# Performance work log

Measured on AMD Instinct MI355X. Metric: run time of the kernel, lower is better.

The kernel has to match this reference:

```python
import jax, jax.numpy as jnp
import numpy as np

HEADS = 4
EPS = 1e-5

def _layernorm(x, g, b):
    mu = jnp.mean(x, axis=-1, keepdims=True)
    var = jnp.var(x, axis=-1, keepdims=True)
    return (x - mu) / jnp.sqrt(var + EPS) * g + b

def setup_inputs() -> dict:
    key = jax.random.key(0)
    ks = jax.random.split(key, 16)
    N, dim, k, G = 400000, 256, 1, 4096
    h = jax.random.normal(ks[0], (N, dim), dtype=jnp.float32)
    batch = jnp.sort(jax.random.randint(ks[1], (N,), 0, G).astype(jnp.int64))
    s = 1.0 / np.sqrt(dim)
    return {
        "h": h,
        "batch": batch,
        "num_graphs": G,
        "seed": jax.random.normal(ks[2], (k, dim), dtype=jnp.float32),
        "in_proj_w": jax.random.uniform(ks[3], (3 * dim, dim), minval=-s, maxval=s, dtype=jnp.float32),
        "in_proj_b": jnp.zeros((3 * dim,), jnp.float32),
        "out_w": jax.random.uniform(ks[4], (dim, dim), minval=-s, maxval=s, dtype=jnp.float32),
        "out_b": jnp.zeros((dim,), jnp.float32),
        "w1": jax.random.uniform(ks[5], (4 * dim, dim), minval=-s, maxval=s, dtype=jnp.float32),
        "b1": jnp.zeros((4 * dim,), jnp.float32),
        "w2": jax.random.uniform(ks[6], (dim, 4 * dim), minval=-1.0 / np.sqrt(4 * dim), maxval=1.0 / np.sqrt(4 * dim), dtype=jnp.float32),
        "b2": jnp.zeros((dim,), jnp.float32),
        "g1": jnp.ones((dim,), jnp.float32),
        "beta1": jnp.zeros((dim,), jnp.float32),
        "g2": jnp.ones((dim,), jnp.float32),
        "beta2": jnp.zeros((dim,), jnp.float32),
    }

def reference(h, batch, num_graphs, seed, in_proj_w, in_proj_b, out_w, out_b,
              w1, b1, w2, b2, g1, beta1, g2, beta2):
    N, dim = h.shape
    k = seed.shape[0]
    hd = dim // HEADS
    G = num_graphs
    # q/k/v projections (torch MHA packed in_proj: rows [0:dim]=Q, [dim:2dim]=K, [2dim:]=V)
    q = seed @ in_proj_w[:dim].T + in_proj_b[:dim]                 # [k, dim]
    kk = h @ in_proj_w[dim:2 * dim].T + in_proj_b[dim:2 * dim]     # [N, dim]
    vv = h @ in_proj_w[2 * dim:].T + in_proj_b[2 * dim:]           # [N, dim]
    qh = q.reshape(k, HEADS, hd).transpose(1, 0, 2)                # [H, k, hd]
    kh = kk.reshape(N, HEADS, hd)                                  # [N, H, hd]
    vh = vv.reshape(N, HEADS, hd)                                  # [N, H, hd]
    scale = 1.0 / np.sqrt(hd)
    scores = jnp.einsum('hkd,nhd->nhk', qh, kh) * scale            # [N, H, k]
    # segment softmax over nodes of each graph
    smax = jax.ops.segment_max(scores, batch, num_segments=G)      # [G, H, k]
    e = jnp.exp(scores - smax[batch])                              # [N, H, k]
    denom = jax.ops.segment_sum(e, batch, num_segments=G)          # [G, H, k]
    wv = jax.ops.segment_sum(e[:, :, :, None] * vh[:, :, None, :], batch, num_segments=G)  # [G, H, k, hd]
    attn = jnp.where(denom[..., None] > 0, wv / jnp.maximum(denom, 1e-9)[..., None], 0.0)
    attn = attn.transpose(0, 2, 1, 3).reshape(G, k, dim)           # [G, k, dim]
    o = attn @ out_w.T + out_b                                     # [G, k, dim]
    x = _layernorm(o + seed[None, :, :], g1, beta1)
    f = jax.nn.relu(x @ w1.T + b1) @ w2.T + b2
    x = _layernorm(x + f, g2, beta2)
    # empty graphs output zeros (matches torch loop)
    count = jax.ops.segment_sum(jnp.ones((N,), jnp.float32), batch, num_segments=G)
    return jnp.where((count > 0)[:, None, None], x, 0.0)
```

## Files before the change

kernel.cpp:

```cpp
#include <hip/hip_runtime.h>
#include <hip/hip_bf16.h>


#define DIM 256
#define CHUNK 16

typedef short bf16x8 __attribute__((ext_vector_type(8)));
typedef float f32x4  __attribute__((ext_vector_type(4)));
#define MFMA16(a, b, c) __builtin_amdgcn_mfma_f32_16x16x32_bf16(a, b, c, 0, 0, 0)

#define GLOAD_LDS16(gp, lp)                                          \
    __builtin_amdgcn_global_load_lds(                                \
        (const __attribute__((address_space(1))) void*)(gp),         \
        (__attribute__((address_space(3))) void*)(lp), 16, 0, 0)

#define OFF_C      0
#define OFF_D      1024
#define OFF_CONST  1040
#define OFF_P2B    2048
#define OFF_W1B    133120
#define OFF_W2B    264192
#define OFF_TB     395264
#define OFF_CNT    6162432
#define OFF_STARTS 6166528

__global__ __launch_bounds__(256) void prep_all_kernel(
    const float* __restrict__ seed, const float* __restrict__ ipw,
    const float* __restrict__ ipb, const float* __restrict__ out_w,
    const float* __restrict__ out_b, const float* __restrict__ w1,
    const float* __restrict__ w2, const int* __restrict__ batch,
    float* __restrict__ cvec, float* __restrict__ dconst,
    float* __restrict__ constvec, __hip_bfloat16* __restrict__ P2b,
    __hip_bfloat16* __restrict__ w1b, __hip_bfloat16* __restrict__ w2b,
    int* __restrict__ starts, int N, int G)
{
    int b = blockIdx.x, t = threadIdx.x;
    __shared__ float q_s[DIM];
    if (b < 1024) {
        int i = b >> 2, hD = b & 3;
        float a = 0.f;
        for (int j = 0; j < 64; ++j)
            a += out_w[i * DIM + hD * 64 + j]
               * ipw[(size_t)(2 * DIM + hD * 64 + j) * DIM + t];
        P2b[(size_t)i * 1024 + hD * DIM + t] = __float2bfloat16(a);
    } else if (b == 1024) {
        const float scale = 0.125f;
        float acc = ipb[t];
        for (int d = 0; d < DIM; ++d) acc += seed[d] * ipw[t * DIM + d];
        q_s[t] = acc;
        __syncthreads();
        for (int hh = 0; hh < 4; ++hh) {
            float a = 0.f;
            for (int j = 0; j < 64; ++j)
                a += q_s[hh * 64 + j] * ipw[(size_t)(DIM + hh * 64 + j) * DIM + t];
            cvec[hh * DIM + t] = a * scale;
        }
        if (t < 4) {
            float a = 0.f;
            for (int j = 0; j < 64; ++j)
                a += q_s[t * 64 + j] * ipb[DIM + t * 64 + j];
            dconst[t] = a * scale;
        }
        float cc = out_b[t];
        for (int c = 0; c < DIM; ++c)
            cc += out_w[t * DIM + c] * ipb[2 * DIM + c];
        constvec[t] = cc;
    } else if (b < 1153) {
        int base = (b - 1025) * 2048 + t;
        for (int i = 0; i < 8; ++i)
            w1b[base + i * 256] = __float2bfloat16(w1[base + i * 256]);
    } else if (b < 1281) {
        int base = (b - 1153) * 2048 + t;
        for (int i = 0; i < 8; ++i)
            w2b[base + i * 256] = __float2bfloat16(w2[base + i * 256]);
    } else {
        int n = (b - 1281) * 256 + t;
        if (n < N) {
            int bn = batch[n];
            int bp = (n == 0) ? -1 : batch[n - 1];
            for (int gg = bp + 1; gg <= bn; ++gg) starts[gg] = n;
            if (n == N - 1)
                for (int gg = bn + 1; gg <= G; ++gg) starts[gg] = N;
        }
    }
}

__global__ __launch_bounds__(256) void attn_pool_kernel(
    const float* __restrict__ hmat, const int* __restrict__ starts,
    const float* __restrict__ cvec, const float* __restrict__ dconst,
    __hip_bfloat16* __restrict__ Tb, int* __restrict__ cnt)
{
    int g = blockIdx.x;
    int tid = threadIdx.x;
    int lane = tid & 63, wave = tid >> 6;

    __shared__ float hbuf[2][CHUNK][DIM];
    __shared__ float lred[4][4];

    int s = starts[g], e = starts[g + 1];
    if (tid == 0) cnt[g] = e - s;
    size_t tbase = (size_t)g * 1024;
    if (e == s) {
        __hip_bfloat16 z = __float2bfloat16(0.f);
        Tb[tbase + tid] = z; Tb[tbase + 256 + tid] = z;
        Tb[tbase + 512 + tid] = z; Tb[tbase + 768 + tid] = z;
        return;
    }

    int hh = lane & 3, seg = lane >> 2;
    const float* cb = cvec + hh * DIM + seg * 16;
    float4 cr0 = *(const float4*)(cb + 0);
    float4 cr1 = *(const float4*)(cb + 4);
    float4 cr2 = *(const float4*)(cb + 8);
    float4 cr3 = *(const float4*)(cb + 12);
    float dc_mine = dconst[hh];

    float S00 = 0.f, S01 = 0.f, S02 = 0.f, S03 = 0.f;
    float S10 = 0.f, S11 = 0.f, S12 = 0.f, S13 = 0.f;
    float S20 = 0.f, S21 = 0.f, S22 = 0.f, S23 = 0.f;
    float S30 = 0.f, S31 = 0.f, S32 = 0.f, S33 = 0.f;
    float lp = 0.f;

    {
        int c0 = min(CHUNK, e - s);
#pragma unroll
        for (int i = 0; i < 4; ++i) {
            int r = wave * 4 + i;
            if (r < c0)
                GLOAD_LDS16(&hmat[(size_t)(s + r) * DIM + lane * 4],
                            &hbuf[0][r][0]);
        }
    }

    int cur = 0;
    for (int n0 = s; n0 < e; n0 += CHUNK, cur ^= 1) {
        int ccnt = min(CHUNK, e - n0);
        __syncthreads();

        int n1 = n0 + CHUNK;
        if (n1 < e) {
            int cn = min(CHUNK, e - n1);
#pragma unroll
            for (int i = 0; i < 4; ++i) {
                int r = wave * 4 + i;
                if (r < cn)
                    GLOAD_LDS16(&hmat[(size_t)(n1 + r) * DIM + lane * 4],
                                &hbuf[cur ^ 1][r][0]);
            }
        }

        for (int j = wave; j < ccnt; j += 4) {
            const float* hb = &hbuf[cur][j][0];
            const float* hs = hb + seg * 16;
            float4 h0 = *(const float4*)(hs + 0);
            float4 h1 = *(const float4*)(hs + 4);
            float4 h2 = *(const float4*)(hs + 8);
            float4 h3 = *(const float4*)(hs + 12);
            float p = h0.x * cr0.x + h0.y * cr0.y + h0.z * cr0.z + h0.w * cr0.w
                    + h1.x * cr1.x + h1.y * cr1.y + h1.z * cr1.z + h1.w * cr1.w
                    + h2.x * cr2.x + h2.y * cr2.y + h2.z * cr2.z + h2.w * cr2.w
                    + h3.x * cr3.x + h3.y * cr3.y + h3.z * cr3.z + h3.w * cr3.w;
            p += __shfl_xor(p, 4);
            p += __shfl_xor(p, 8);
            p += __shfl_xor(p, 16);
            p += __shfl_xor(p, 32);
            float ev = __expf(p + dc_mine);
            lp += ev;
            float e0 = __shfl(ev, 0), e1 = __shfl(ev, 1);
            float e2 = __shfl(ev, 2), e3 = __shfl(ev, 3);
            float v0 = hb[lane], v1 = hb[64 + lane];
            float v2 = hb[128 + lane], v3 = hb[192 + lane];
            S00 = fmaf(e0, v0, S00); S01 = fmaf(e0, v1, S01);
            S02 = fmaf(e0, v2, S02); S03 = fmaf(e0, v3, S03);
            S10 = fmaf(e1, v0, S10); S11 = fmaf(e1, v1, S11);
            S12 = fmaf(e1, v2, S12); S13 = fmaf(e1, v3, S13);
            S20 = fmaf(e2, v0, S20); S21 = fmaf(e2, v1, S21);
            S22 = fmaf(e2, v2, S22); S23 = fmaf(e2, v3, S23);
            S30 = fmaf(e3, v0, S30); S31 = fmaf(e3, v1, S31);
            S32 = fmaf(e3, v2, S32); S33 = fmaf(e3, v3, S33);
        }
    }

    __syncthreads();
    float* part = &hbuf[0][0][0];
#define PIDX(w_, h_, c_) ((((w_) * 4 + (h_)) * 4 + (c_)) * 64 + lane)
    part[PIDX(wave, 0, 0)] = S00; part[PIDX(wave, 0, 1)] = S01;
    part[PIDX(wave, 0, 2)] = S02; part[PIDX(wave, 0, 3)] = S03;
    part[PIDX(wave, 1, 0)] = S10; part[PIDX(wave, 1, 1)] = S11;
    part[PIDX(wave, 1, 2)] = S12; part[PIDX(wave, 1, 3)] = S13;
    part[PIDX(wave, 2, 0)] = S20; part[PIDX(wave, 2, 1)] = S21;
    part[PIDX(wave, 2, 2)] = S22; part[PIDX(wave, 2, 3)] = S23;
    part[PIDX(wave, 3, 0)] = S30; part[PIDX(wave, 3, 1)] = S31;
    part[PIDX(wave, 3, 2)] = S32; part[PIDX(wave, 3, 3)] = S33;
#undef PIDX
    if (lane < 4) lred[wave][lane] = lp;
    __syncthreads();

    int cg = tid >> 6, ln = tid & 63;
#pragma unroll
    for (int h = 0; h < 4; ++h) {
        int base = (h * 4 + cg) * 64 + ln;
        float sum = part[base] + part[base + 1024]
                  + part[base + 2048] + part[base + 3072];
        float den = lred[0][h] + lred[1][h] + lred[2][h] + lred[3][h];
        Tb[tbase + h * 256 + tid] = __float2bfloat16(sum / den);
    }
}

__global__ __launch_bounds__(256) void mlp_fused_kernel(
    const __hip_bfloat16* __restrict__ Tb, const __hip_bfloat16* __restrict__ P2b,
    const float* __restrict__ constvec, const float* __restrict__ seed,
    const float* __restrict__ g1, const float* __restrict__ be1,
    const __hip_bfloat16* __restrict__ w1b, const float* __restrict__ b1,
    const __hip_bfloat16* __restrict__ w2b, const float* __restrict__ b2,
    const float* __restrict__ g2, const float* __restrict__ be2,
    const int* __restrict__ cnt, float* __restrict__ outp)
{
    int m0 = blockIdx.x * 16;
    int tid = threadIdx.x;
    int w = tid >> 6, lane = tid & 63, quad = lane >> 4, l16 = lane & 15;

    __shared__ float x1s[16][260];
    __shared__ __hip_bfloat16 x1bs[16][264];
    __shared__ __hip_bfloat16 us[16][1032];
    __shared__ float redS[4][16], redQ[4][16];

    f32x4 acc0[4];
#pragma unroll
    for (int i = 0; i < 4; ++i) acc0[i] = (f32x4){0.f, 0.f, 0.f, 0.f};
    const __hip_bfloat16* Ap0 = Tb + (size_t)(m0 + l16) * 1024 + quad * 8;
    const __hip_bfloat16* Bp0 = P2b + (size_t)(w * 64 + l16) * 1024 + quad * 8;
    for (int k0 = 0; k0 < 1024; k0 += 32) {
        bf16x8 a = *(const bf16x8*)(Ap0 + k0);
#pragma unroll
        for (int nt = 0; nt < 4; ++nt) {
            bf16x8 b = *(const bf16x8*)(Bp0 + (size_t)nt * 16 * 1024 + k0);
            acc0[nt] = MFMA16(a, b, acc0[nt]);
        }
    }
    float v0[4][4];
    {
        float sum[4] = {0, 0, 0, 0}, sq[4] = {0, 0, 0, 0};
#pragma unroll
        for (int nt = 0; nt < 4; ++nt) {
            int col = w * 64 + nt * 16 + l16;
            float cv = constvec[col] + seed[col];
#pragma unroll
            for (int r = 0; r < 4; ++r) {
                float x = acc0[nt][r] + cv;
                v0[nt][r] = x; sum[r] += x; sq[r] += x * x;
            }
        }
#pragma unroll
        for (int r = 0; r < 4; ++r) {
            float s_ = sum[r], q_ = sq[r];
            s_ += __shfl_xor(s_, 1);  q_ += __shfl_xor(q_, 1);
            s_ += __shfl_xor(s_, 2);  q_ += __shfl_xor(q_, 2);
            s_ += __shfl_xor(s_, 4);  q_ += __shfl_xor(q_, 4);
            s_ += __shfl_xor(s_, 8);  q_ += __shfl_xor(q_, 8);
            if (l16 == 0) { redS[w][quad * 4 + r] = s_; redQ[w][quad * 4 + r] = q_; }
        }
    }
    __syncthreads();
    {
        float mu_r[4], rs_r[4];
#pragma unroll
        for (int r = 0; r < 4; ++r) {
            int row = quad * 4 + r;
            float s_ = redS[0][row] + redS[1][row] + redS[2][row] + redS[3][row];
            float q_ = redQ[0][row] + redQ[1][row] + redQ[2][row] + redQ[3][row];
            float mu = s_ * (1.f / 256);
            float var = q_ * (1.f / 256) - mu * mu;
            mu_r[r] = mu;
            rs_r[r] = rsqrtf(fmaxf(var, 0.f) + 1e-5f);
        }
#pragma unroll
        for (int nt = 0; nt < 4; ++nt) {
            int col = w * 64 + nt * 16 + l16;
            float gg = g1[col], bb = be1[col];
#pragma unroll
            for (int r = 0; r < 4; ++r) {
                int row = quad * 4 + r;
                float y = (v0[nt][r] - mu_r[r]) * rs_r[r] * gg + bb;
                x1s[row][col] = y;
                x1bs[row][col] = __float2bfloat16(y);
            }
        }
    }
    __syncthreads();

    f32x4 acc1[16];
#pragma unroll
    for (int i = 0; i < 16; ++i) acc1[i] = (f32x4){0.f, 0.f, 0.f, 0.f};
    const __hip_bfloat16* Bp1 = w1b + (size_t)(w * 256 + l16) * 256 + quad * 8;
#pragma unroll
    for (int k0 = 0; k0 < 256; k0 += 32) {
        bf16x8 a = *(const bf16x8*)&x1bs[l16][quad * 8 + k0];
#pragma unroll
        for (int nt = 0; nt < 16; ++nt) {
            bf16x8 b = *(const bf16x8*)(Bp1 + (size_t)nt * 16 * 256 + k0);
            acc1[nt] = MFMA16(a, b, acc1[nt]);
        }
    }
#pragma unroll
    for (int nt = 0; nt < 16; ++nt) {
        int col = w * 256 + nt * 16 + l16;
        float bb = b1[col];
#pragma unroll
        for (int r = 0; r < 4; ++r) {
            int row = quad * 4 + r;
            us[row][col] = __float2bfloat16(fmaxf(acc1[nt][r] + bb, 0.f));
        }
    }
    __syncthreads();

    f32x4 acc2[4];
#pragma unroll
    for (int i = 0; i < 4; ++i) acc2[i] = (f32x4){0.f, 0.f, 0.f, 0.f};
    const __hip_bfloat16* Bp2 = w2b + (size_t)(w * 64 + l16) * 1024 + quad * 8;
    for (int k0 = 0; k0 < 1024; k0 += 32) {
        bf16x8 a = *(const bf16x8*)&us[l16][quad * 8 + k0];
#pragma unroll
        for (int nt = 0; nt < 4; ++nt) {
            bf16x8 b = *(const bf16x8*)(Bp2 + (size_t)nt * 16 * 1024 + k0);
            acc2[nt] = MFMA16(a, b, acc2[nt]);
        }
    }
    float v2[4][4];
    {
        float sum[4] = {0, 0, 0, 0}, sq[4] = {0, 0, 0, 0};
#pragma unroll
        for (int nt = 0; nt < 4; ++nt) {
            int col = w * 64 + nt * 16 + l16;
            float bb = b2[col];
#pragma unroll
            for (int r = 0; r < 4; ++r) {
                int row = quad * 4 + r;
                float x = acc2[nt][r] + bb + x1s[row][col];
                v2[nt][r] = x; sum[r] += x; sq[r] += x * x;
            }
        }
#pragma unroll
        for (int r = 0; r < 4; ++r) {
            float s_ = sum[r], q_ = sq[r];
            s_ += __shfl_xor(s_, 1);  q_ += __shfl_xor(q_, 1);
            s_ += __shfl_xor(s_, 2);  q_ += __shfl_xor(q_, 2);
            s_ += __shfl_xor(s_, 4);  q_ += __shfl_xor(q_, 4);
            s_ += __shfl_xor(s_, 8);  q_ += __shfl_xor(q_, 8);
            if (l16 == 0) { redS[w][quad * 4 + r] = s_; redQ[w][quad * 4 + r] = q_; }
        }
    }
    __syncthreads();
    {
#pragma unroll
        for (int r = 0; r < 4; ++r) {
            int row = quad * 4 + r;
            float s_ = redS[0][row] + redS[1][row] + redS[2][row] + redS[3][row];
            float q_ = redQ[0][row] + redQ[1][row] + redQ[2][row] + redQ[3][row];
            float mu = s_ * (1.f / 256);
            float var = q_ * (1.f / 256) - mu * mu;
            float rs = rsqrtf(fmaxf(var, 0.f) + 1e-5f);
            int gr = m0 + row;
            float mask = (cnt[gr] > 0) ? 1.f : 0.f;
#pragma unroll
            for (int nt = 0; nt < 4; ++nt) {
                int col = w * 64 + nt * 16 + l16;
                float y = ((v2[nt][r] - mu) * rs * g2[col] + be2[col]) * mask;
                outp[(size_t)gr * 256 + col] = y;
            }
        }
    }
}

extern "C" void kernel_launch(void* const* d_in, const int* in_sizes, int n_in,
                              void* d_out, int out_size, void* d_ws, size_t ws_size,
                              hipStream_t stream) {
    const float* h     = (const float*)d_in[0];
    const int*   batch = (const int*)d_in[1];
    const float* seed  = (const float*)d_in[3];
    const float* ipw   = (const float*)d_in[4];
    const float* ipb   = (const float*)d_in[5];
    const float* out_w = (const float*)d_in[6];
    const float* out_b = (const float*)d_in[7];
    const float* w1    = (const float*)d_in[8];
    const float* b1    = (const float*)d_in[9];
    const float* w2    = (const float*)d_in[10];
    const float* b2    = (const float*)d_in[11];
    const float* g1    = (const float*)d_in[12];
    const float* be1   = (const float*)d_in[13];
    const float* g2    = (const float*)d_in[14];
    const float* be2   = (const float*)d_in[15];

    int N = in_sizes[1];
    int G = out_size / DIM;

    float* ws = (float*)d_ws;
    float* cvec     = ws + OFF_C;
    float* dconst   = ws + OFF_D;
    float* constvec = ws + OFF_CONST;
    __hip_bfloat16* P2b = (__hip_bfloat16*)(ws + OFF_P2B);
    __hip_bfloat16* w1b = (__hip_bfloat16*)(ws + OFF_W1B);
    __hip_bfloat16* w2b = (__hip_bfloat16*)(ws + OFF_W2B);
    __hip_bfloat16* Tb  = (__hip_bfloat16*)(ws + OFF_TB);
    int*   cnt      = (int*)(ws + OFF_CNT);
    int*   startsp  = (int*)(ws + OFF_STARTS);

    int sblocks = (N + 255) / 256;
    prep_all_kernel<<<1281 + sblocks, 256, 0, stream>>>(
        seed, ipw, ipb, out_w, out_b, w1, w2, batch,
        cvec, dconst, constvec, P2b, w1b, w2b, startsp, N, G);
    attn_pool_kernel<<<G, 256, 0, stream>>>(h, startsp, cvec, dconst, Tb, cnt);
    mlp_fused_kernel<<<G / 16, 256, 0, stream>>>(Tb, P2b, constvec, seed, g1, be1,
                                                 w1b, b1, w2b, b2, g2, be2, cnt,
                                                 (float*)d_out);
}
```

Baseline: 663.7 us.

## Use per-wave private LDS buffers in attention pool, widen MLP block to 16 waves

The attention pooling kernel now gives each wave its own double-buffered LDS rows. It issues next-chunk loads unconditionally, clamping row indices, and waits with s_waitcnt vmcnt instead of block-wide __syncthreads, which removes barrier stalls in the streaming loop. The MLP kernel goes from 4 to 16 waves per block, each computing a narrower slice of columns, to raise parallelism and latency hiding for the small 256-block grid. The costs are redundant clamped loads on tail chunks, reliance on manual waitcnt correctness, and larger LayerNorm cross-wave reductions over 16 partials.

```diff
diff --git a/kernel.cpp b/kernel.cpp
--- a/kernel.cpp
+++ b/kernel.cpp
@@ -94,7 +94,7 @@
     int tid = threadIdx.x;
     int lane = tid & 63, wave = tid >> 6;
 
-    __shared__ float hbuf[2][CHUNK][DIM];
+    __shared__ float hbuf[4][2][4][DIM];
     __shared__ float lred[4][4];
 
     int s = starts[g], e = starts[g + 1];
@@ -121,36 +121,30 @@
     float S30 = 0.f, S31 = 0.f, S32 = 0.f, S33 = 0.f;
     float lp = 0.f;
 
-    {
-        int c0 = min(CHUNK, e - s);
-#pragma unroll
-        for (int i = 0; i < 4; ++i) {
-            int r = wave * 4 + i;
-            if (r < c0)
-                GLOAD_LDS16(&hmat[(size_t)(s + r) * DIM + lane * 4],
-                            &hbuf[0][r][0]);
-        }
+    int rows0 = wave * 4;
+
+#pragma unroll
+    for (int i = 0; i < 4; ++i) {
+        int r = min(s + rows0 + i, e - 1);
+        GLOAD_LDS16(&hmat[(size_t)r * DIM + lane * 4], &hbuf[wave][0][i][0]);
     }
 
     int cur = 0;
     for (int n0 = s; n0 < e; n0 += CHUNK, cur ^= 1) {
         int ccnt = min(CHUNK, e - n0);
-        __syncthreads();
-
         int n1 = n0 + CHUNK;
-        if (n1 < e) {
-            int cn = min(CHUNK, e - n1);
-#pragma unroll
-            for (int i = 0; i < 4; ++i) {
-                int r = wave * 4 + i;
-                if (r < cn)
-                    GLOAD_LDS16(&hmat[(size_t)(n1 + r) * DIM + lane * 4],
-                                &hbuf[cur ^ 1][r][0]);
-            }
-        }
-
-        for (int j = wave; j < ccnt; j += 4) {
-            const float* hb = &hbuf[cur][j][0];
+#pragma unroll
+        for (int i = 0; i < 4; ++i) {
+            int r = min(n1 + rows0 + i, e - 1);
+            GLOAD_LDS16(&hmat[(size_t)r * DIM + lane * 4],
+                        &hbuf[wave][cur ^ 1][i][0]);
+        }
+        asm volatile("s_waitcnt vmcnt(4)" ::: "memory");
+        __builtin_amdgcn_sched_barrier(0);
+
+        int nmine = min(max(ccnt - rows0, 0), 4);
+        for (int j = 0; j < nmine; ++j) {
+            const float* hb = &hbuf[wave][cur][j][0];
             const float* hs = hb + seg * 16;
             float4 h0 = *(const float4*)(hs + 0);
             float4 h1 = *(const float4*)(hs + 4);
@@ -181,8 +175,10 @@
         }
     }
 
-    __syncthreads();
-    float* part = &hbuf[0][0][0];
+    asm volatile("s_waitcnt vmcnt(0)" ::: "memory");
+    __builtin_amdgcn_sched_barrier(0);
+    __syncthreads();
+    float* part = &hbuf[0][0][0][0];
 #define PIDX(w_, h_, c_) ((((w_) * 4 + (h_)) * 4 + (c_)) * 64 + lane)
     part[PIDX(wave, 0, 0)] = S00; part[PIDX(wave, 0, 1)] = S01;
     part[PIDX(wave, 0, 2)] = S02; part[PIDX(wave, 0, 3)] = S03;
@@ -207,7 +203,7 @@
     }
 }
 
-__global__ __launch_bounds__(256) void mlp_fused_kernel(
+__global__ __launch_bounds__(1024) void mlp_fused_kernel(
     const __hip_bfloat16* __restrict__ Tb, const __hip_bfloat16* __restrict__ P2b,
     const float* __restrict__ constvec, const float* __restrict__ seed,
     const float* __restrict__ g1, const float* __restrict__ be1,
@@ -223,33 +219,26 @@
     __shared__ float x1s[16][260];
     __shared__ __hip_bfloat16 x1bs[16][264];
     __shared__ __hip_bfloat16 us[16][1032];
-    __shared__ float redS[4][16], redQ[4][16];
-
-    f32x4 acc0[4];
-#pragma unroll
-    for (int i = 0; i < 4; ++i) acc0[i] = (f32x4){0.f, 0.f, 0.f, 0.f};
+    __shared__ float redS[16][16], redQ[16][16];
+
+    f32x4 acc0 = (f32x4){0.f, 0.f, 0.f, 0.f};
     const __hip_bfloat16* Ap0 = Tb + (size_t)(m0 + l16) * 1024 + quad * 8;
-    const __hip_bfloat16* Bp0 = P2b + (size_t)(w * 64 + l16) * 1024 + quad * 8;
+    const __hip_bfloat16* Bp0 = P2b + (size_t)(w * 16 + l16) * 1024 + quad * 8;
+#pragma unroll 4
     for (int k0 = 0; k0 < 1024; k0 += 32) {
         bf16x8 a = *(const bf16x8*)(Ap0 + k0);
-#pragma unroll
-        for (int nt = 0; nt < 4; ++nt) {
-            bf16x8 b = *(const bf16x8*)(Bp0 + (size_t)nt * 16 * 1024 + k0);
-            acc0[nt] = MFMA16(a, b, acc0[nt]);
-        }
-    }
-    float v0[4][4];
+        bf16x8 b = *(const bf16x8*)(Bp0 + k0);
+        acc0 = MFMA16(a, b, acc0);
+    }
+    float v0[4];
     {
-        float sum[4] = {0, 0, 0, 0}, sq[4] = {0, 0, 0, 0};
-#pragma unroll
-        for (int nt = 0; nt < 4; ++nt) {
-            int col = w * 64 + nt * 16 + l16;
-            float cv = constvec[col] + seed[col];
-#pragma unroll
-            for (int r = 0; r < 4; ++r) {
-                float x = acc0[nt][r] + cv;
-                v0[nt][r] = x; sum[r] += x; sq[r] += x * x;
-            }
+        int col = w * 16 + l16;
+        float cv = constvec[col] + seed[col];
+        float sum[4], sq[4];
+#pragma unroll
+        for (int r = 0; r < 4; ++r) {
+            float x = acc0[r] + cv;
+            v0[r] = x; sum[r] = x; sq[r] = x * x;
         }
 #pragma unroll
         for (int r = 0; r < 4; ++r) {
@@ -267,44 +256,42 @@
 #pragma unroll
         for (int r = 0; r < 4; ++r) {
             int row = quad * 4 + r;
-            float s_ = redS[0][row] + redS[1][row] + redS[2][row] + redS[3][row];
-            float q_ = redQ[0][row] + redQ[1][row] + redQ[2][row] + redQ[3][row];
+            float s_ = 0.f, q_ = 0.f;
+#pragma unroll
+            for (int ww = 0; ww < 16; ++ww) { s_ += redS[ww][row]; q_ += redQ[ww][row]; }
             float mu = s_ * (1.f / 256);
             float var = q_ * (1.f / 256) - mu * mu;
             mu_r[r] = mu;
             rs_r[r] = rsqrtf(fmaxf(var, 0.f) + 1e-5f);
         }
-#pragma unroll
-        for (int nt = 0; nt < 4; ++nt) {
-            int col = w * 64 + nt * 16 + l16;
-            float gg = g1[col], bb = be1[col];
-#pragma unroll
-            for (int r = 0; r < 4; ++r) {
-                int row = quad * 4 + r;
-                float y = (v0[nt][r] - mu_r[r]) * rs_r[r] * gg + bb;
-                x1s[row][col] = y;
-                x1bs[row][col] = __float2bfloat16(y);
-            }
-        }
-    }
-    __syncthreads();
-
-    f32x4 acc1[16];
-#pragma unroll
-    for (int i = 0; i < 16; ++i) acc1[i] = (f32x4){0.f, 0.f, 0.f, 0.f};
-    const __hip_bfloat16* Bp1 = w1b + (size_t)(w * 256 + l16) * 256 + quad * 8;
+        int col = w * 16 + l16;
+        float gg = g1[col], bb = be1[col];
+#pragma unroll
+        for (int r = 0; r < 4; ++r) {
+            int row = quad * 4 + r;
+            float y = (v0[r] - mu_r[r]) * rs_r[r] * gg + bb;
+            x1s[row][col] = y;
+            x1bs[row][col] = __float2bfloat16(y);
+        }
+    }
+    __syncthreads();
+
+    f32x4 acc1[4];
+#pragma unroll
+    for (int i = 0; i < 4; ++i) acc1[i] = (f32x4){0.f, 0.f, 0.f, 0.f};
+    const __hip_bfloat16* Bp1 = w1b + (size_t)(w * 64 + l16) * 256 + quad * 8;
 #pragma unroll
     for (int k0 = 0; k0 < 256; k0 += 32) {
         bf16x8 a = *(const bf16x8*)&x1bs[l16][quad * 8 + k0];
 #pragma unroll
-        for (int nt = 0; nt < 16; ++nt) {
+        for (int nt = 0; nt < 4; ++nt) {
             bf16x8 b = *(const bf16x8*)(Bp1 + (size_t)nt * 16 * 256 + k0);
             acc1[nt] = MFMA16(a, b, acc1[nt]);
         }
     }
 #pragma unroll
-    for (int nt = 0; nt < 16; ++nt) {
-        int col = w * 256 + nt * 16 + l16;
+    for (int nt = 0; nt < 4; ++nt) {
+        int col = w * 64 + nt * 16 + l16;
         float bb = b1[col];
 #pragma unroll
         for (int r = 0; r < 4; ++r) {
@@ -314,31 +301,24 @@
     }
     __syncthreads();
 
-    f32x4 acc2[4];
-#pragma unroll
-    for (int i = 0; i < 4; ++i) acc2[i] = (f32x4){0.f, 0.f, 0.f, 0.f};
-    const __hip_bfloat16* Bp2 = w2b + (size_t)(w * 64 + l16) * 1024 + quad * 8;
+    f32x4 acc2 = (f32x4){0.f, 0.f, 0.f, 0.f};
+    const __hip_bfloat16* Bp2 = w2b + (size_t)(w * 16 + l16) * 1024 + quad * 8;
+#pragma unroll 4
     for (int k0 = 0; k0 < 1024; k0 += 32) {
         bf16x8 a = *(const bf16x8*)&us[l16][quad * 8 + k0];
-#pragma unroll
-        for (int nt = 0; nt < 4; ++nt) {
-            bf16x8 b = *(const bf16x8*)(Bp2 + (size_t)nt * 16 * 1024 + k0);
-            acc2[nt] = MFMA16(a, b, acc2[nt]);
-        }
-    }
-    float v2[4][4];
+        bf16x8 b = *(const bf16x8*)(Bp2 + k0);
+        acc2 = MFMA16(a, b, acc2);
+    }
+    float v2[4];
     {
-        float sum[4] = {0, 0, 0, 0}, sq[4] = {0, 0, 0, 0};
-#pragma unroll
-        for (int nt = 0; nt < 4; ++nt) {
-            int col = w * 64 + nt * 16 + l16;
-            float bb = b2[col];
-#pragma unroll
-            for (int r = 0; r < 4; ++r) {
-                int row = quad * 4 + r;
-                float x = acc2[nt][r] + bb + x1s[row][col];
-                v2[nt][r] = x; sum[r] += x; sq[r] += x * x;
-            }
+        int col = w * 16 + l16;
+        float bb = b2[col];
+        float sum[4], sq[4];
+#pragma unroll
+        for (int r = 0; r < 4; ++r) {
+            int row = quad * 4 + r;
+            float x = acc2[r] + bb + x1s[row][col];
+            v2[r] = x; sum[r] = x; sq[r] = x * x;
         }
 #pragma unroll
         for (int r = 0; r < 4; ++r) {
@@ -352,22 +332,21 @@
     }
     __syncthreads();
     {
-#pragma unroll
-        for (int r = 0; r < 4; ++r) {
-            int row = quad * 4 + r;
-            float s_ = redS[0][row] + redS[1][row] + redS[2][row] + redS[3][row];
-            float q_ = redQ[0][row] + redQ[1][row] + redQ[2][row] + redQ[3][row];
+        int col = w * 16 + l16;
+        float gg = g2[col], bb = be2[col];
+#pragma unroll
+        for (int r = 0; r < 4; ++r) {
+            int row = quad * 4 + r;
+            float s_ = 0.f, q_ = 0.f;
+#pragma unroll
+            for (int ww = 0; ww < 16; ++ww) { s_ += redS[ww][row]; q_ += redQ[ww][row]; }
             float mu = s_ * (1.f / 256);
             float var = q_ * (1.f / 256) - mu * mu;
             float rs = rsqrtf(fmaxf(var, 0.f) + 1e-5f);
             int gr = m0 + row;
             float mask = (cnt[gr] > 0) ? 1.f : 0.f;
-#pragma unroll
-            for (int nt = 0; nt < 4; ++nt) {
-                int col = w * 64 + nt * 16 + l16;
-                float y = ((v2[nt][r] - mu) * rs * g2[col] + be2[col]) * mask;
-                outp[(size_t)gr * 256 + col] = y;
-            }
+            float y = ((v2[r] - mu) * rs * gg + bb) * mask;
+            outp[(size_t)gr * 256 + col] = y;
         }
     }
 }
@@ -410,7 +389,7 @@
         seed, ipw, ipb, out_w, out_b, w1, w2, batch,
         cvec, dconst, constvec, P2b, w1b, w2b, startsp, N, G);
     attn_pool_kernel<<<G, 256, 0, stream>>>(h, startsp, cvec, dconst, Tb, cnt);
-    mlp_fused_kernel<<<G / 16, 256, 0, stream>>>(Tb, P2b, constvec, seed, g1, be1,
-                                                 w1b, b1, w2b, b2, g2, be2, cnt,
-                                                 (float*)d_out);
+    mlp_fused_kernel<<<G / 16, 1024, 0, stream>>>(Tb, P2b, constvec, seed, g1, be1,
+                                                  w1b, b1, w2b, b2, g2, be2, cnt,
+                                                  (float*)d_out);
 }
```

New measurement: 666.0 us. No clear change (+0.3%).
